# Optimization experiments

Measured on AMD Instinct MI355X. Metric: run time of the kernel, lower is better.

## Reference

```python
import jax, jax.numpy as jnp
import numpy as np

B, N, EPG, D, V = 512, 100, 1600, 128, 20215
K1, K2 = 80, 64  # ceil(0.8*100), ceil(0.8*80)


def setup_inputs() -> dict:
    key = jax.random.key(0)
    ks = jax.random.split(key, 14)
    x_idx = jax.random.randint(ks[0], (B * N,), 0, V)
    off = (jnp.arange(B) * N)[:, None]
    src = (jax.random.randint(ks[1], (B, EPG), 0, N) + off).reshape(-1)
    dst = (jax.random.randint(ks[2], (B, EPG), 0, N) + off).reshape(-1)
    edge_index = jnp.stack([src, dst])
    batch = jnp.repeat(jnp.arange(B), N)
    s = 1.0 / np.sqrt(D)
    return {
        "x_idx": x_idx,
        "edge_index": edge_index,
        "batch": batch,
        "emb": jax.random.normal(ks[3], (V, D), jnp.float32),
        "Wl": jax.random.normal(ks[4], (D, D), jnp.float32) * s,
        "bl": jnp.zeros((D,), jnp.float32),
        "Wr": jax.random.normal(ks[5], (D, D), jnp.float32) * s,
        "pw1": jax.random.normal(ks[6], (D,), jnp.float32) * s,
        "pw2": jax.random.normal(ks[7], (D,), jnp.float32) * s,
        "W1": jax.random.normal(ks[8], (2 * D, 64), jnp.float32) * (1.0 / np.sqrt(2 * D)),
        "b1": jnp.zeros((64,), jnp.float32),
        "W3": jax.random.normal(ks[9], (64, 1), jnp.float32) * 0.125,
        "b3": jnp.zeros((1,), jnp.float32),
    }


def _topk_pool(h, w, k):
    # h: [B, n, D]; PyG TopKPooling: score = tanh((h @ w)/||w||), keep top-k, scale by score
    score = jnp.tanh(jnp.einsum("bnd,d->bn", h, w) / jnp.linalg.norm(w))
    vals, idx = jax.lax.top_k(score, k)  # [B, k]
    hp = jnp.take_along_axis(h, idx[..., None], axis=1) * vals[..., None]
    return hp


def _readout(hp):
    # global max pool || global mean pool -> [B, 2D]
    return jnp.concatenate([hp.max(axis=1), hp.mean(axis=1)], axis=-1)


def reference(x_idx, edge_index, batch, emb, Wl, bl, Wr, pw1, pw2, W1, b1, W3, b3):
    Nt = x_idx.shape[0]
    h = emb[x_idx]  # [Nt, D]
    src, dst = edge_index[0], edge_index[1]
    # SAGEConv: mean-aggregate source features at destinations
    agg = jax.ops.segment_sum(h[src], dst, num_segments=Nt)
    deg = jax.ops.segment_sum(jnp.ones((src.shape[0],), h.dtype), dst, num_segments=Nt)
    mean = agg / jnp.maximum(deg, 1.0)[:, None]
    h = jax.nn.relu(mean @ Wl + bl + h @ Wr)

    hg = h.reshape(B, N, D)
    hp1 = _topk_pool(hg, pw1, K1)   # [B, K1, D]
    x1 = _readout(hp1)              # [B, 2D]
    hp2 = _topk_pool(hp1, pw2, K2)  # [B, K2, D]
    x2 = _readout(hp2)

    x = x1 + x2
    x = jax.nn.relu(x @ W1 + b1)
    # dropout is identity in eval mode
    out = jax.nn.sigmoid(x @ W3 + b3).squeeze(-1)  # [B]
    return out
```

## Files before the change

kernel.cpp:

```cpp
#include <hip/hip_runtime.h>
#include <hip/hip_bf16.h>
#include <math.h>

#define BGRAPH 512
#define NNODE  100
#define EPG    1600
#define DIM    128
#define ETOT   (BGRAPH * EPG)
#define PAD    132
#define K1     80
#define K2     64
#define NTHREADS 1024

typedef __attribute__((ext_vector_type(8))) short short8;
typedef __attribute__((ext_vector_type(4))) float f32x4;

__device__ __forceinline__ ushort bf16_rne(float x) {
    unsigned u = __float_as_uint(x);
    u += 0x7FFFu + ((u >> 16) & 1u);
    return (ushort)(u >> 16);
}
__device__ __forceinline__ float bf16f(ushort h) {
    return __uint_as_float(((unsigned)h) << 16);
}

__global__ __launch_bounds__(256) void wprep(const float* __restrict__ Wl,
                                             const float* __restrict__ Wr,
                                             ushort* __restrict__ whi,
                                             ushort* __restrict__ wlo) {
    int t = blockIdx.x * 256 + threadIdx.x;
    if (t >= 8 * 8 * 64) return;
    int lane = t & 63, ks = (t >> 6) & 7, nt = t >> 9;
    int n  = nt * 16 + (lane & 15);
    int kb = ks * 32 + 8 * (lane >> 4);
#pragma unroll
    for (int j = 0; j < 8; ++j) {
        int k = kb + j;
        float w = (k < 128) ? Wl[k * 128 + n] : Wr[(k - 128) * 128 + n];
        ushort hi = bf16_rne(w);
        whi[t * 8 + j] = hi;
        wlo[t * 8 + j] = bf16_rne(w - bf16f(hi));
    }
}

__global__ __launch_bounds__(NTHREADS) void fused_gnn(
    const int*   __restrict__ x_idx,
    const int*   __restrict__ edge_index,
    const float* __restrict__ emb,
    const float* __restrict__ blv,
    const float* __restrict__ pw1,
    const float* __restrict__ pw2,
    const float* __restrict__ W1,
    const float* __restrict__ b1g,
    const float* __restrict__ W3,
    const float* __restrict__ b3g,
    const ushort* __restrict__ whi,
    const ushort* __restrict__ wlo,
    float*       __restrict__ out)
{
    __shared__ __align__(16) float h0[128 * PAD];
    __shared__ __align__(16) int   acnt[128 * PAD];
    __shared__ int degi[NNODE];
    __shared__ int nid[NNODE];
    __shared__ float score1[NNODE], q2[NNODE], s2v[NNODE];
    __shared__ int   rank1[NNODE], rank2[NNODE];
    __shared__ float xv[2 * DIM];

    float* meanF = reinterpret_cast<float*>(acnt);

    const int g    = blockIdx.x;
    const int tid  = threadIdx.x;
    const int lane = tid & 63;
    const int wv   = tid >> 6;

    {
        int4* a4 = reinterpret_cast<int4*>(acnt);
        for (int i = tid; i < 128 * PAD / 4; i += NTHREADS) a4[i] = int4{0, 0, 0, 0};
        float4* hz = reinterpret_cast<float4*>(h0 + 100 * PAD);
        for (int i = tid; i < 28 * PAD / 4; i += NTHREADS) hz[i] = float4{0, 0, 0, 0};
        if (tid < NNODE) { nid[tid] = x_idx[g * NNODE + tid]; degi[tid] = 0; }
    }
    __syncthreads();

    {
        const float4* emb4 = reinterpret_cast<const float4*>(emb);
        for (int i = tid; i < NNODE * 32; i += NTHREADS) {
            int n = i >> 5, q = i & 31;
            float4 v = emb4[nid[n] * 32 + q];
            *reinterpret_cast<float4*>(&h0[n * PAD + q * 4]) = v;
        }
        for (int i = tid; i < EPG; i += NTHREADS) {
            int s = edge_index[g * EPG + i] - g * NNODE;
            int d = edge_index[ETOT + g * EPG + i] - g * NNODE;
            atomicAdd(&acnt[d * PAD + s], 1);
            atomicAdd(&degi[d], 1);
        }
    }
    __syncthreads();

    const int mg = wv >> 2, ng = wv & 3;

    {
        f32x4 acc[2][2];
#pragma unroll
        for (int im = 0; im < 2; ++im)
#pragma unroll
            for (int in = 0; in < 2; ++in) acc[im][in] = f32x4{0.f, 0.f, 0.f, 0.f};

        for (int ks = 0; ks < 4; ++ks) {
            const int kb = ks * 32 + 8 * (lane >> 4);
            short8 a[2];
#pragma unroll
            for (int im = 0; im < 2; ++im) {
                int row = (2 * mg + im) * 16 + (lane & 15);
                const int* s = &acnt[row * PAD + kb];
                int4 u0 = *reinterpret_cast<const int4*>(s);
                int4 u1 = *reinterpret_cast<const int4*>(s + 4);
                int vi[8] = {u0.x, u0.y, u0.z, u0.w, u1.x, u1.y, u1.z, u1.w};
#pragma unroll
                for (int j = 0; j < 8; ++j) a[im][j] = (short)bf16_rne((float)vi[j]);
            }
            short8 bh[2], bl2[2];
#pragma unroll
            for (int in = 0; in < 2; ++in) {
                int n = (2 * ng + in) * 16 + (lane & 15);
#pragma unroll
                for (int j = 0; j < 8; ++j) {
                    float v = h0[(kb + j) * PAD + n];
                    ushort hb = bf16_rne(v);
                    bh[in][j]  = (short)hb;
                    bl2[in][j] = (short)bf16_rne(v - bf16f(hb));
                }
            }
#pragma unroll
            for (int im = 0; im < 2; ++im)
#pragma unroll
                for (int in = 0; in < 2; ++in) {
                    acc[im][in] = __builtin_amdgcn_mfma_f32_16x16x32_bf16(a[im], bh[in],  acc[im][in], 0, 0, 0);
                    acc[im][in] = __builtin_amdgcn_mfma_f32_16x16x32_bf16(a[im], bl2[in], acc[im][in], 0, 0, 0);
                }
        }
        __syncthreads();
#pragma unroll
        for (int im = 0; im < 2; ++im) {
            int rbase = (2 * mg + im) * 16 + 4 * (lane >> 4);
#pragma unroll
            for (int in = 0; in < 2; ++in) {
                int col = (2 * ng + in) * 16 + (lane & 15);
#pragma unroll
                for (int r = 0; r < 4; ++r) {
                    int row = rbase + r;
                    if (row < NNODE) {
                        float invd = 1.0f / fmaxf((float)degi[row], 1.0f);
                        meanF[row * PAD + col] = acc[im][in][r] * invd;
                    }
                }
            }
        }
    }
    __syncthreads();

    {
        f32x4 acc[2][2];
#pragma unroll
        for (int im = 0; im < 2; ++im)
#pragma unroll
            for (int in = 0; in < 2; ++in) acc[im][in] = f32x4{0.f, 0.f, 0.f, 0.f};

        for (int ks = 0; ks < 8; ++ks) {
            const float* Xs = (ks < 4) ? meanF : h0;
            const int kb = (ks & 3) * 32 + 8 * (lane >> 4);
            short8 ah[2], al[2];
#pragma unroll
            for (int im = 0; im < 2; ++im) {
                int row = (2 * mg + im) * 16 + (lane & 15);
                const float* s = &Xs[row * PAD + kb];
                float4 v0 = *reinterpret_cast<const float4*>(s);
                float4 v1 = *reinterpret_cast<const float4*>(s + 4);
                float vf[8] = {v0.x, v0.y, v0.z, v0.w, v1.x, v1.y, v1.z, v1.w};
#pragma unroll
                for (int j = 0; j < 8; ++j) {
                    ushort hb = bf16_rne(vf[j]);
                    ah[im][j] = (short)hb;
                    al[im][j] = (short)bf16_rne(vf[j] - bf16f(hb));
                }
            }
            short8 bh[2], bl2[2];
#pragma unroll
            for (int in = 0; in < 2; ++in) {
                int t = ((2 * ng + in) * 8 + ks) * 64 + lane;
                bh[in]  = *reinterpret_cast<const short8*>(whi + (size_t)t * 8);
                bl2[in] = *reinterpret_cast<const short8*>(wlo + (size_t)t * 8);
            }
#pragma unroll
            for (int im = 0; im < 2; ++im)
#pragma unroll
                for (int in = 0; in < 2; ++in) {
                    acc[im][in] = __builtin_amdgcn_mfma_f32_16x16x32_bf16(ah[im], bh[in],  acc[im][in], 0, 0, 0);
                    acc[im][in] = __builtin_amdgcn_mfma_f32_16x16x32_bf16(al[im], bh[in],  acc[im][in], 0, 0, 0);
                    acc[im][in] = __builtin_amdgcn_mfma_f32_16x16x32_bf16(ah[im], bl2[in], acc[im][in], 0, 0, 0);
                }
        }
        __syncthreads();
#pragma unroll
        for (int im = 0; im < 2; ++im) {
            int rbase = (2 * mg + im) * 16 + 4 * (lane >> 4);
#pragma unroll
            for (int in = 0; in < 2; ++in) {
                int col = (2 * ng + in) * 16 + (lane & 15);
                float bc = blv[col];
#pragma unroll
                for (int r = 0; r < 4; ++r) {
                    int row = rbase + r;
                    if (row < NNODE)
                        h0[row * PAD + col] = fmaxf(acc[im][in][r] + bc, 0.0f);
                }
            }
        }
    }
    __syncthreads();

    {
        float a1 = pw1[lane], c1 = pw1[lane + 64];
        float a2 = pw2[lane], c2 = pw2[lane + 64];
        float n1 = a1 * a1 + c1 * c1;
        float n2 = a2 * a2 + c2 * c2;
#pragma unroll
        for (int off = 32; off; off >>= 1) {
            n1 += __shfl_xor(n1, off);
            n2 += __shfl_xor(n2, off);
        }
        float rn1 = 1.0f / sqrtf(n1);
        float rn2 = 1.0f / sqrtf(n2);

        for (int n = wv; n < NNODE; n += 16) {
            float hA = h0[n * PAD + lane], hB = h0[n * PAD + lane + 64];
            float d1 = hA * a1 + hB * c1;
            float d2 = hA * a2 + hB * c2;
#pragma unroll
            for (int off = 32; off; off >>= 1) {
                d1 += __shfl_xor(d1, off);
                d2 += __shfl_xor(d2, off);
            }
            if (lane == 0) {
                score1[n] = tanhf(d1 * rn1);
                q2[n]     = d2 * rn2;
            }
        }
    }
    __syncthreads();

    if (tid < NNODE) {
        float si = score1[tid];
        int r = 0;
        for (int j = 0; j < NNODE; ++j) {
            float sj = score1[j];
            r += (sj > si || (sj == si && j < tid)) ? 1 : 0;
        }
        rank1[tid] = r;
        s2v[tid] = tanhf(score1[tid] * q2[tid]);
    }
    __syncthreads();

    if (tid < NNODE) {
        int r1i = rank1[tid];
        if (r1i < K1) {
            float si = s2v[tid];
            int r = 0;
            for (int j = 0; j < NNODE; ++j) {
                if (rank1[j] < K1) {
                    float sj = s2v[j];
                    r += (sj > si || (sj == si && rank1[j] < r1i)) ? 1 : 0;
                }
            }
            rank2[tid] = r;
        } else {
            rank2[tid] = 1 << 30;
        }
    }
    __syncthreads();

    {
        float* redm1 = meanF;
        float* reds1 = meanF + 1024;
        float* redm2 = meanF + 2048;
        float* reds2 = meanF + 3072;
        int f = tid & 127;
        int c = tid >> 7;
        float mx1 = -INFINITY, sm1 = 0.0f, mx2 = -INFINITY, sm2 = 0.0f;
        for (int n = c; n < NNODE; n += 8) {
            if (rank1[n] < K1) {
                float v1 = h0[n * PAD + f] * score1[n];
                mx1 = fmaxf(mx1, v1);
                sm1 += v1;
                if (rank2[n] < K2) {
                    float v2 = v1 * s2v[n];
                    mx2 = fmaxf(mx2, v2);
                    sm2 += v2;
                }
            }
        }
        redm1[c * DIM + f] = mx1; reds1[c * DIM + f] = sm1;
        redm2[c * DIM + f] = mx2; reds2[c * DIM + f] = sm2;
        __syncthreads();
        if (tid < DIM) {
            float m1 = -INFINITY, s1 = 0.0f, m2 = -INFINITY, s2 = 0.0f;
#pragma unroll
            for (int cc = 0; cc < 8; ++cc) {
                m1 = fmaxf(m1, redm1[cc * DIM + tid]); s1 += reds1[cc * DIM + tid];
                m2 = fmaxf(m2, redm2[cc * DIM + tid]); s2 += reds2[cc * DIM + tid];
            }
            xv[tid]       = m1 + m2;
            xv[DIM + tid] = s1 * (1.0f / K1) + s2 * (1.0f / K2);
        }
    }
    __syncthreads();

    {
        float* part = meanF + 4096;
        int o = tid & 63, ch = tid >> 6;
        float acc = 0.0f;
#pragma unroll
        for (int u = 0; u < 16; ++u) {
            int f = ch * 16 + u;
            acc += xv[f] * W1[f * 64 + o];
        }
        part[ch * 64 + o] = acc;
        __syncthreads();
        if (tid < 64) {
            float a2 = b1g[tid];
#pragma unroll
            for (int cc = 0; cc < 16; ++cc) a2 += part[cc * 64 + tid];
            float y = fmaxf(a2, 0.0f);
            float r = y * W3[tid];
#pragma unroll
            for (int off = 32; off; off >>= 1) r += __shfl_xor(r, off);
            if (tid == 0) out[g] = 1.0f / (1.0f + expf(-(r + b3g[0])));
        }
    }
}

extern "C" void kernel_launch(void* const* d_in, const int* in_sizes, int n_in,
                              void* d_out, int out_size, void* d_ws, size_t ws_size,
                              hipStream_t stream) {
    const int*   x_idx      = (const int*)d_in[0];
    const int*   edge_index = (const int*)d_in[1];
    const float* emb = (const float*)d_in[3];
    const float* Wl  = (const float*)d_in[4];
    const float* bl  = (const float*)d_in[5];
    const float* Wr  = (const float*)d_in[6];
    const float* pw1 = (const float*)d_in[7];
    const float* pw2 = (const float*)d_in[8];
    const float* W1  = (const float*)d_in[9];
    const float* b1  = (const float*)d_in[10];
    const float* W3  = (const float*)d_in[11];
    const float* b3  = (const float*)d_in[12];
    float* out = (float*)d_out;

    ushort* whi = (ushort*)d_ws;
    ushort* wlo = (ushort*)((char*)d_ws + 65536);

    wprep<<<16, 256, 0, stream>>>(Wl, Wr, whi, wlo);
    fused_gnn<<<BGRAPH, NTHREADS, 0, stream>>>(
        x_idx, edge_index, emb, bl, pw1, pw2, W1, b1, W3, b3, whi, wlo, out);
}
```

Measured before the change: 158.1 us.

## Reassociate SAGE aggregation as A·(H·Wl) with pre-packed bf16 fragments

Reorders the SAGEConv computation: it first computes H·Wl and H·Wr with split-bf16 MFMAs, then multiplies the edge-count adjacency by the H·Wl product and applies the degree normalization in the epilogue. H and the adjacency counts are converted once into MFMA fragment layout in shared memory, which removes the per-iteration bf16 conversion and the strided column loads of the old first GEMM. The adjacency GEMM now uses two MFMAs per tile instead of three passes over a mean matrix. It adds an extra shared-memory repacking pass and extra syncs, and it rounds the intermediate H·Wl to split bf16, so numerics shift slightly.

```diff
diff --git a/kernel.cpp b/kernel.cpp
--- a/kernel.cpp
+++ b/kernel.cpp
@@ -13,6 +13,7 @@
 #define NTHREADS 1024
 
 typedef __attribute__((ext_vector_type(8))) short short8;
+typedef __attribute__((ext_vector_type(4))) short short4v;
 typedef __attribute__((ext_vector_type(4))) float f32x4;
 
 __device__ __forceinline__ ushort bf16_rne(float x) {
@@ -42,6 +43,7 @@
         wlo[t * 8 + j] = bf16_rne(w - bf16f(hi));
     }
 }
+
 
 __global__ __launch_bounds__(NTHREADS) void fused_gnn(
     const int*   __restrict__ x_idx,
@@ -58,26 +60,25 @@
     const ushort* __restrict__ wlo,
     float*       __restrict__ out)
 {
-    __shared__ __align__(16) float h0[128 * PAD];
-    __shared__ __align__(16) int   acnt[128 * PAD];
+    __shared__ __align__(16) float Xf[128 * PAD];
+    __shared__ __align__(16) int   Zi[128 * PAD];
     __shared__ int degi[NNODE];
     __shared__ int nid[NNODE];
     __shared__ float score1[NNODE], q2[NNODE], s2v[NNODE];
     __shared__ int   rank1[NNODE], rank2[NNODE];
     __shared__ float xv[2 * DIM];
 
-    float* meanF = reinterpret_cast<float*>(acnt);
-
     const int g    = blockIdx.x;
     const int tid  = threadIdx.x;
     const int lane = tid & 63;
     const int wv   = tid >> 6;
-
-    {
-        int4* a4 = reinterpret_cast<int4*>(acnt);
-        for (int i = tid; i < 128 * PAD / 4; i += NTHREADS) a4[i] = int4{0, 0, 0, 0};
-        float4* hz = reinterpret_cast<float4*>(h0 + 100 * PAD);
-        for (int i = tid; i < 28 * PAD / 4; i += NTHREADS) hz[i] = float4{0, 0, 0, 0};
+    const int mg = wv >> 2, ng = wv & 3;
+
+    {
+        int4* z4 = reinterpret_cast<int4*>(Zi);
+        for (int i = tid; i < 128 * PAD / 4; i += NTHREADS) z4[i] = int4{0, 0, 0, 0};
+        float4* xz = reinterpret_cast<float4*>(Xf + 100 * PAD);
+        for (int i = tid; i < 28 * PAD / 4; i += NTHREADS) xz[i] = float4{0, 0, 0, 0};
         if (tid < NNODE) { nid[tid] = x_idx[g * NNODE + tid]; degi[tid] = 0; }
     }
     __syncthreads();
@@ -87,133 +88,163 @@
         for (int i = tid; i < NNODE * 32; i += NTHREADS) {
             int n = i >> 5, q = i & 31;
             float4 v = emb4[nid[n] * 32 + q];
-            *reinterpret_cast<float4*>(&h0[n * PAD + q * 4]) = v;
+            *reinterpret_cast<float4*>(&Xf[n * PAD + q * 4]) = v;
         }
         for (int i = tid; i < EPG; i += NTHREADS) {
             int s = edge_index[g * EPG + i] - g * NNODE;
             int d = edge_index[ETOT + g * EPG + i] - g * NNODE;
-            atomicAdd(&acnt[d * PAD + s], 1);
+            atomicAdd(&Zi[d * PAD + s], 1);
             atomicAdd(&degi[d], 1);
         }
     }
     __syncthreads();
 
-    const int mg = wv >> 2, ng = wv & 3;
-
-    {
-        f32x4 acc[2][2];
+    ushort* ahhi = reinterpret_cast<ushort*>(Xf);
+    ushort* ahlo = ahhi + 16384;
+    ushort* abf  = reinterpret_cast<ushort*>(Zi);
+
+    {
+        const int m  = tid >> 3;
+        const int kb = (tid & 7) * 16;
+        float hv[16];
+        int   cv[16];
+#pragma unroll
+        for (int u = 0; u < 4; ++u) {
+            float4 v = *reinterpret_cast<const float4*>(&Xf[m * PAD + kb + 4 * u]);
+            hv[4 * u] = v.x; hv[4 * u + 1] = v.y; hv[4 * u + 2] = v.z; hv[4 * u + 3] = v.w;
+            int4 c = *reinterpret_cast<const int4*>(&Zi[m * PAD + kb + 4 * u]);
+            cv[4 * u] = c.x; cv[4 * u + 1] = c.y; cv[4 * u + 2] = c.z; cv[4 * u + 3] = c.w;
+        }
+        __syncthreads();
+#pragma unroll
+        for (int g2 = 0; g2 < 2; ++g2) {
+            int idx = ((m >> 4) * 4 + (kb >> 5)) * 512 +
+                      ((m & 15) + 16 * (((kb >> 3) + g2) & 3)) * 8;
+            short8 hh, hl, ab;
+#pragma unroll
+            for (int j = 0; j < 8; ++j) {
+                float v = hv[g2 * 8 + j];
+                ushort hb = bf16_rne(v);
+                hh[j] = (short)hb;
+                hl[j] = (short)bf16_rne(v - bf16f(hb));
+                ab[j] = (short)bf16_rne((float)cv[g2 * 8 + j]);
+            }
+            *reinterpret_cast<short8*>(&ahhi[idx]) = hh;
+            *reinterpret_cast<short8*>(&ahlo[idx]) = hl;
+            *reinterpret_cast<short8*>(&abf[idx])  = ab;
+        }
+    }
+    __syncthreads();
+
+    f32x4 accP[2][2], accQ[2][2];
+#pragma unroll
+    for (int im = 0; im < 2; ++im)
+#pragma unroll
+        for (int in = 0; in < 2; ++in) {
+            accP[im][in] = f32x4{0.f, 0.f, 0.f, 0.f};
+            accQ[im][in] = f32x4{0.f, 0.f, 0.f, 0.f};
+        }
+#pragma unroll
+    for (int ks = 0; ks < 4; ++ks) {
+        short8 Ah[2], Al[2];
+#pragma unroll
+        for (int im = 0; im < 2; ++im) {
+            int fi = (((2 * mg + im) * 4 + ks) * 64 + lane) * 8;
+            Ah[im] = *reinterpret_cast<const short8*>(&ahhi[fi]);
+            Al[im] = *reinterpret_cast<const short8*>(&ahlo[fi]);
+        }
+        short8 BhL[2], BlL[2], BhR[2], BlR[2];
+#pragma unroll
+        for (int in = 0; in < 2; ++in) {
+            int nt = 2 * ng + in;
+            int tL = ((nt * 8 + ks) * 64 + lane) * 8;
+            int tR = ((nt * 8 + ks + 4) * 64 + lane) * 8;
+            BhL[in] = *reinterpret_cast<const short8*>(whi + tL);
+            BlL[in] = *reinterpret_cast<const short8*>(wlo + tL);
+            BhR[in] = *reinterpret_cast<const short8*>(whi + tR);
+            BlR[in] = *reinterpret_cast<const short8*>(wlo + tR);
+        }
 #pragma unroll
         for (int im = 0; im < 2; ++im)
 #pragma unroll
-            for (int in = 0; in < 2; ++in) acc[im][in] = f32x4{0.f, 0.f, 0.f, 0.f};
-
-        for (int ks = 0; ks < 4; ++ks) {
-            const int kb = ks * 32 + 8 * (lane >> 4);
-            short8 a[2];
-#pragma unroll
-            for (int im = 0; im < 2; ++im) {
-                int row = (2 * mg + im) * 16 + (lane & 15);
-                const int* s = &acnt[row * PAD + kb];
-                int4 u0 = *reinterpret_cast<const int4*>(s);
-                int4 u1 = *reinterpret_cast<const int4*>(s + 4);
-                int vi[8] = {u0.x, u0.y, u0.z, u0.w, u1.x, u1.y, u1.z, u1.w};
-#pragma unroll
-                for (int j = 0; j < 8; ++j) a[im][j] = (short)bf16_rne((float)vi[j]);
-            }
-            short8 bh[2], bl2[2];
-#pragma unroll
             for (int in = 0; in < 2; ++in) {
-                int n = (2 * ng + in) * 16 + (lane & 15);
-#pragma unroll
-                for (int j = 0; j < 8; ++j) {
-                    float v = h0[(kb + j) * PAD + n];
-                    ushort hb = bf16_rne(v);
-                    bh[in][j]  = (short)hb;
-                    bl2[in][j] = (short)bf16_rne(v - bf16f(hb));
-                }
-            }
-#pragma unroll
-            for (int im = 0; im < 2; ++im)
-#pragma unroll
-                for (int in = 0; in < 2; ++in) {
-                    acc[im][in] = __builtin_amdgcn_mfma_f32_16x16x32_bf16(a[im], bh[in],  acc[im][in], 0, 0, 0);
-                    acc[im][in] = __builtin_amdgcn_mfma_f32_16x16x32_bf16(a[im], bl2[in], acc[im][in], 0, 0, 0);
-                }
-        }
-        __syncthreads();
+                accP[im][in] = __builtin_amdgcn_mfma_f32_16x16x32_bf16(Ah[im], BhL[in], accP[im][in], 0, 0, 0);
+                accP[im][in] = __builtin_amdgcn_mfma_f32_16x16x32_bf16(Al[im], BhL[in], accP[im][in], 0, 0, 0);
+                accP[im][in] = __builtin_amdgcn_mfma_f32_16x16x32_bf16(Ah[im], BlL[in], accP[im][in], 0, 0, 0);
+                accQ[im][in] = __builtin_amdgcn_mfma_f32_16x16x32_bf16(Ah[im], BhR[in], accQ[im][in], 0, 0, 0);
+                accQ[im][in] = __builtin_amdgcn_mfma_f32_16x16x32_bf16(Al[im], BhR[in], accQ[im][in], 0, 0, 0);
+                accQ[im][in] = __builtin_amdgcn_mfma_f32_16x16x32_bf16(Ah[im], BlR[in], accQ[im][in], 0, 0, 0);
+            }
+    }
+    __syncthreads();
+
+    {
+        ushort* pbhi = ahhi;
+        ushort* pblo = ahlo;
 #pragma unroll
         for (int im = 0; im < 2; ++im) {
-            int rbase = (2 * mg + im) * 16 + 4 * (lane >> 4);
+            int row0 = (2 * mg + im) * 16 + 4 * (lane >> 4);
 #pragma unroll
             for (int in = 0; in < 2; ++in) {
                 int col = (2 * ng + in) * 16 + (lane & 15);
+                int idx = ((col >> 4) * 4 + (row0 >> 5)) * 512 +
+                          ((col & 15) + 16 * ((row0 >> 3) & 3)) * 8 + (row0 & 7);
+                short4v h4, l4;
 #pragma unroll
                 for (int r = 0; r < 4; ++r) {
-                    int row = rbase + r;
-                    if (row < NNODE) {
-                        float invd = 1.0f / fmaxf((float)degi[row], 1.0f);
-                        meanF[row * PAD + col] = acc[im][in][r] * invd;
-                    }
+                    float v = accP[im][in][r];
+                    ushort hb = bf16_rne(v);
+                    h4[r] = (short)hb;
+                    l4[r] = (short)bf16_rne(v - bf16f(hb));
                 }
-            }
-        }
-    }
-    __syncthreads();
-
-    {
-        f32x4 acc[2][2];
+                *reinterpret_cast<short4v*>(&pbhi[idx]) = h4;
+                *reinterpret_cast<short4v*>(&pblo[idx]) = l4;
+            }
+        }
+    }
+    __syncthreads();
+
+    f32x4 accR[2][2];
+#pragma unroll
+    for (int im = 0; im < 2; ++im)
+#pragma unroll
+        for (int in = 0; in < 2; ++in) accR[im][in] = f32x4{0.f, 0.f, 0.f, 0.f};
+#pragma unroll
+    for (int ks = 0; ks < 4; ++ks) {
+        short8 Ab[2];
 #pragma unroll
         for (int im = 0; im < 2; ++im)
-#pragma unroll
-            for (int in = 0; in < 2; ++in) acc[im][in] = f32x4{0.f, 0.f, 0.f, 0.f};
-
-        for (int ks = 0; ks < 8; ++ks) {
-            const float* Xs = (ks < 4) ? meanF : h0;
-            const int kb = (ks & 3) * 32 + 8 * (lane >> 4);
-            short8 ah[2], al[2];
-#pragma unroll
-            for (int im = 0; im < 2; ++im) {
-                int row = (2 * mg + im) * 16 + (lane & 15);
-                const float* s = &Xs[row * PAD + kb];
-                float4 v0 = *reinterpret_cast<const float4*>(s);
-                float4 v1 = *reinterpret_cast<const float4*>(s + 4);
-                float vf[8] = {v0.x, v0.y, v0.z, v0.w, v1.x, v1.y, v1.z, v1.w};
-#pragma unroll
-                for (int j = 0; j < 8; ++j) {
-                    ushort hb = bf16_rne(vf[j]);
-                    ah[im][j] = (short)hb;
-                    al[im][j] = (short)bf16_rne(vf[j] - bf16f(hb));
-                }
-            }
-            short8 bh[2], bl2[2];
+            Ab[im] = *reinterpret_cast<const short8*>(&abf[(((2 * mg + im) * 4 + ks) * 64 + lane) * 8]);
+        short8 Bh[2], Bl[2];
+#pragma unroll
+        for (int in = 0; in < 2; ++in) {
+            int fi = (((2 * ng + in) * 4 + ks) * 64 + lane) * 8;
+            Bh[in] = *reinterpret_cast<const short8*>(&ahhi[fi]);
+            Bl[in] = *reinterpret_cast<const short8*>(&ahlo[fi]);
+        }
+#pragma unroll
+        for (int im = 0; im < 2; ++im)
 #pragma unroll
             for (int in = 0; in < 2; ++in) {
-                int t = ((2 * ng + in) * 8 + ks) * 64 + lane;
-                bh[in]  = *reinterpret_cast<const short8*>(whi + (size_t)t * 8);
-                bl2[in] = *reinterpret_cast<const short8*>(wlo + (size_t)t * 8);
-            }
-#pragma unroll
-            for (int im = 0; im < 2; ++im)
-#pragma unroll
-                for (int in = 0; in < 2; ++in) {
-                    acc[im][in] = __builtin_amdgcn_mfma_f32_16x16x32_bf16(ah[im], bh[in],  acc[im][in], 0, 0, 0);
-                    acc[im][in] = __builtin_amdgcn_mfma_f32_16x16x32_bf16(al[im], bh[in],  acc[im][in], 0, 0, 0);
-                    acc[im][in] = __builtin_amdgcn_mfma_f32_16x16x32_bf16(ah[im], bl2[in], acc[im][in], 0, 0, 0);
-                }
-        }
-        __syncthreads();
-#pragma unroll
-        for (int im = 0; im < 2; ++im) {
-            int rbase = (2 * mg + im) * 16 + 4 * (lane >> 4);
-#pragma unroll
-            for (int in = 0; in < 2; ++in) {
-                int col = (2 * ng + in) * 16 + (lane & 15);
-                float bc = blv[col];
-#pragma unroll
-                for (int r = 0; r < 4; ++r) {
-                    int row = rbase + r;
-                    if (row < NNODE)
-                        h0[row * PAD + col] = fmaxf(acc[im][in][r] + bc, 0.0f);
+                accR[im][in] = __builtin_amdgcn_mfma_f32_16x16x32_bf16(Ab[im], Bh[in], accR[im][in], 0, 0, 0);
+                accR[im][in] = __builtin_amdgcn_mfma_f32_16x16x32_bf16(Ab[im], Bl[in], accR[im][in], 0, 0, 0);
+            }
+    }
+    __syncthreads();
+
+#pragma unroll
+    for (int im = 0; im < 2; ++im) {
+        int rbase = (2 * mg + im) * 16 + 4 * (lane >> 4);
+#pragma unroll
+        for (int in = 0; in < 2; ++in) {
+            int col = (2 * ng + in) * 16 + (lane & 15);
+            float bc = blv[col];
+#pragma unroll
+            for (int r = 0; r < 4; ++r) {
+                int row = rbase + r;
+                if (row < NNODE) {
+                    float invd = 1.0f / fmaxf((float)degi[row], 1.0f);
+                    Xf[row * PAD + col] = fmaxf(accR[im][in][r] * invd + accQ[im][in][r] + bc, 0.0f);
                 }
             }
         }
@@ -234,7 +265,7 @@
         float rn2 = 1.0f / sqrtf(n2);
 
         for (int n = wv; n < NNODE; n += 16) {
-            float hA = h0[n * PAD + lane], hB = h0[n * PAD + lane + 64];
+            float hA = Xf[n * PAD + lane], hB = Xf[n * PAD + lane + 64];
             float d1 = hA * a1 + hB * c1;
             float d2 = hA * a2 + hB * c2;
 #pragma unroll
@@ -281,16 +312,17 @@
     __syncthreads();
 
     {
-        float* redm1 = meanF;
-        float* reds1 = meanF + 1024;
-        float* redm2 = meanF + 2048;
-        float* reds2 = meanF + 3072;
+        float* Zf = reinterpret_cast<float*>(Zi);
+        float* redm1 = Zf;
+        float* reds1 = Zf + 1024;
+        float* redm2 = Zf + 2048;
+        float* reds2 = Zf + 3072;
         int f = tid & 127;
         int c = tid >> 7;
         float mx1 = -INFINITY, sm1 = 0.0f, mx2 = -INFINITY, sm2 = 0.0f;
         for (int n = c; n < NNODE; n += 8) {
             if (rank1[n] < K1) {
-                float v1 = h0[n * PAD + f] * score1[n];
+                float v1 = Xf[n * PAD + f] * score1[n];
                 mx1 = fmaxf(mx1, v1);
                 sm1 += v1;
                 if (rank2[n] < K2) {
@@ -317,7 +349,8 @@
     __syncthreads();
 
     {
-        float* part = meanF + 4096;
+        float* Zf = reinterpret_cast<float*>(Zi);
+        float* part = Zf + 4096;
         int o = tid & 63, ch = tid >> 6;
         float acc = 0.0f;
 #pragma unroll
```

Result: faster. 153.9 us (-2.7%).
